# Kernel optimization log

Measured on AMD Instinct MI355X. Metric: run time of the kernel, lower is better.

Reference implementation:

```python
import jax, jax.numpy as jnp
import numpy as np
import math

BASE_RES = 16; SCALE = 1.47; N_LEVELS = 16; FDIM = 2; MAX_SPLASH = 4
LOG2 = 17; HM = 1 << LOG2; SPLITS = [0.9375, 0.875]  # sorted descending as in module


def _build_cfg():
    res = [int(BASE_RES * SCALE ** i) for i in range(N_LEVELS)]
    ns = [0] * N_LEVELS
    for i in range(N_LEVELS):
        for j, s in enumerate(SPLITS):
            if i >= N_LEVELS * s:
                ns[i] = MAX_SPLASH // (2 ** j)
                break
    nidx = [min(r ** 3, HM) for r in res]
    nfeat = [nidx[i] * max(ns[i], 1) for i in range(N_LEVELS)]
    ngau = [nidx[i] * ns[i] for i in range(N_LEVELS)]
    fb = np.concatenate([[0], np.cumsum(nfeat)]).astype(np.int64)
    gb = np.concatenate([[0], np.cumsum(ngau)]).astype(np.int64)
    return res, ns, nidx, fb, gb

RES, NS, NIDX, FB, GB = _build_cfg()
OFFS = np.array([[(k >> 2) & 1, (k >> 1) & 1, k & 1] for k in range(8)], dtype=np.int32)
PRIMES = np.array([1, 2654435761, 805459861], dtype=np.uint32)
SQRT2PI = math.sqrt(2.0 * math.pi)


def _corners_coeffs(coords, res):
    # coords: (N,3) in [0,1). Returns corners (N,8,3) int32 and trilinear coeffs (N,8).
    x = jnp.clip(res * coords, 0.0, res - 1.001)
    pos = jnp.floor(x).astype(jnp.int32)
    xf = x - pos.astype(coords.dtype)
    offs = jnp.asarray(OFFS)
    corners = pos[:, None, :] + offs[None]
    w = jnp.where(offs[None].astype(bool), xf[:, None, :], 1.0 - xf[:, None, :])
    return corners, jnp.prod(w, axis=-1)


def _hash_index(corners, res):
    # linear index if grid fits in table, else xor-prime spatial hash (mod 2^17)
    if res ** 3 <= HM:
        return corners[..., 0] + corners[..., 1] * res + corners[..., 2] * (res * res)
    c = corners.astype(jnp.uint32)
    p = jnp.asarray(PRIMES)
    h = (c[..., 0] * p[0]) ^ (c[..., 1] * p[1]) ^ (c[..., 2] * p[2])
    return (h & jnp.uint32(HM - 1)).astype(jnp.int32)


def setup_inputs() -> dict:
    key = jax.random.key(0)
    k1, k2, k3, k4 = jax.random.split(key, 4)
    N = 262144
    coords = jax.random.uniform(k1, (N, 3), dtype=jnp.float32)
    feats = 0.01 * jax.random.normal(k2, (int(FB[-1]), FDIM), dtype=jnp.float32)
    # means: uniform in a ball of radius 0.25 centered at 0.5 (init_mean)
    G = int(GB[-1])
    pts = jax.random.normal(k3, (G, 3), dtype=jnp.float32)
    r = jnp.sqrt(jax.random.uniform(jax.random.fold_in(k3, 1), (G, 1), dtype=jnp.float32))
    means = pts / jnp.linalg.norm(pts, axis=1, keepdims=True) * r * 0.25 + 0.5
    # stds: N(0.125, 0.02) as in fixed_std=False branch
    stds = 0.125 + 0.02 * jax.random.normal(k4, (G, 1), dtype=jnp.float32)
    return {"coords": coords, "feats": feats, "means": means, "stds": stds}


def reference(coords, feats, means, stds):
    out_feats = []
    out_gmm = []
    for i in range(N_LEVELS):
        res = RES[i]; ns = NS[i]
        corners, coeffs = _corners_coeffs(coords, res)  # (N,8,3), (N,8)
        idx = _hash_index(corners, res)                 # (N,8)
        f = feats[int(FB[i]):int(FB[i + 1])].reshape(-1, max(ns, 1), FDIM)[idx]  # (N,8,S,F)
        if ns:
            m = means[int(GB[i]):int(GB[i + 1])].reshape(-1, ns, 3)[idx]   # (N,8,S,3)
            s = jnp.abs(stds[int(GB[i]):int(GB[i + 1])].reshape(-1, ns, 1)[idx])  # (N,8,S,1)
            diff = coords[:, None, None, :] - m
            sq = jnp.sum(diff * diff / (2.0 * s * s + 1e-7), axis=-1, keepdims=True)
            gw = jnp.exp(-sq) / (SQRT2PI * s + 1e-7)                        # Gaussian weights
            dw = jnp.sum(jnp.abs(diff / s) ** 2, axis=-1, keepdims=True)    # normalized sq dist
            out_feats.append(jnp.einsum('nc,ncsf->nf', coeffs, gw * f))
            out_gmm.append(jnp.einsum('nc,ncs->n', coeffs, (gw * dw)[..., 0]))
        else:
            out_feats.append(jnp.einsum('nc,ncf->nf', coeffs, f[:, :, 0, :]))
    return jnp.concatenate(out_feats, axis=-1), jnp.stack(out_gmm, axis=-1)
```

## Files before the change

### kernel.cpp

```cpp
#include <hip/hip_runtime.h>
#include <math.h>


#define HMASK 131071
typedef float vf4 __attribute__((ext_vector_type(4)));
typedef float vf2 __attribute__((ext_vector_type(2)));
typedef _Float16 h8 __attribute__((ext_vector_type(8)));
typedef unsigned short u16;
typedef unsigned int u32;

#define LIN_OFF 2621440
#define L14_OFF 3670016
#define L15_OFF 7864320

__constant__ int c_fbh[10] = {180567,311639,442711,573783,704855,835927,
                              966999,1098071,1229143,1360215};
__constant__ int c_lres[4] = {16,23,34,50};
__constant__ int c_lfb[4]  = {0,4096,16263,55567};
__constant__ int c_h0res[4] = {74,109,161,237};
__constant__ int c_p1resA[3] = {348,512,753};
__constant__ int c_p1resB[3] = {1108,1629,2394};

__device__ __forceinline__ void corner_setup(int res, float cx, float cy, float cz,
                                             int& px, int& py, int& pz,
                                             float& fx, float& fy, float& fz)
{
    const float hi = (float)res - 1.001f;
    float x = fminf(fmaxf((float)res * cx, 0.0f), hi);
    float y = fminf(fmaxf((float)res * cy, 0.0f), hi);
    float z = fminf(fmaxf((float)res * cz, 0.0f), hi);
    px = (int)x; py = (int)y; pz = (int)z;
    fx = x - (float)px; fy = y - (float)py; fz = z - (float)pz;
}


__device__ __forceinline__ float2 linear_eval4(
    int res, int fbase, float cx, float cy, float cz,
    const float* __restrict__ feats)
{
    int px, py, pz; float fx, fy, fz;
    corner_setup(res, cx, cy, cz, px, py, pz, fx, fy, fz);
    int idxs[4]; float wyz[4];
#pragma unroll
    for (int j = 0; j < 4; ++j) {
        const int oy = (j >> 1) & 1, oz = j & 1;
        idxs[j] = px + (py + oy) * res + (pz + oz) * res * res;
        wyz[j] = (oy ? fy : 1.0f - fy) * (oz ? fz : 1.0f - fz);
    }
    vf4 fv[4];
#pragma unroll
    for (int j = 0; j < 4; ++j)
        fv[j] = *(const vf4*)(feats + (size_t)(fbase + idxs[j]) * 2);
    float a0 = 0.0f, a1 = 0.0f;
    const float gx = 1.0f - fx;
#pragma unroll
    for (int j = 0; j < 4; ++j) {
        a0 += wyz[j] * (gx * fv[j].x + fx * fv[j].z);
        a1 += wyz[j] * (gx * fv[j].y + fx * fv[j].w);
    }
    return make_float2(a0, a1);
}

__device__ __forceinline__ float2 plain_eval_f32h(
    int res, int fbase, float cx, float cy, float cz,
    const float* __restrict__ feats)
{
    int px, py, pz; float fx, fy, fz;
    corner_setup(res, cx, cy, cz, px, py, pz, fx, fy, fz);
    int   idxs[8];
    float ws[8];
#pragma unroll
    for (int k = 0; k < 8; ++k) {
        const int ox = (k >> 2) & 1, oy = (k >> 1) & 1, oz = k & 1;
        const int ix = px + ox, iy = py + oy, iz = pz + oz;
        ws[k] = (ox ? fx : 1.0f - fx) * (oy ? fy : 1.0f - fy) * (oz ? fz : 1.0f - fz);
        unsigned h = (unsigned)ix ^ ((unsigned)iy * 2654435761u) ^ ((unsigned)iz * 805459861u);
        idxs[k] = (int)(h & HMASK);
    }
    float2 fv[8];
#pragma unroll
    for (int k = 0; k < 8; ++k)
        fv[k] = *(const float2*)(feats + (size_t)(fbase + idxs[k]) * 2);
    float a0 = 0.0f, a1 = 0.0f;
#pragma unroll
    for (int k = 0; k < 8; ++k) { a0 += ws[k] * fv[k].x; a1 += ws[k] * fv[k].y; }
    return make_float2(a0, a1);
}


__device__ __forceinline__ float2 linear_eval4_fp8(
    int res, int ebase, float cx, float cy, float cz,
    const u32* __restrict__ ltab)
{
    int px, py, pz; float fx, fy, fz;
    corner_setup(res, cx, cy, cz, px, py, pz, fx, fy, fz);
    int idxs[4]; float wyz[4];
#pragma unroll
    for (int j = 0; j < 4; ++j) {
        const int oy = (j >> 1) & 1, oz = j & 1;
        idxs[j] = px + (py + oy) * res + (pz + oz) * res * res;
        wyz[j] = (oy ? fy : 1.0f - fy) * (oz ? fz : 1.0f - fz);
    }
    u32 u[4];
#pragma unroll
    for (int j = 0; j < 4; ++j) u[j] = ltab[ebase + idxs[j]];
    float a0 = 0.0f, a1 = 0.0f;
    const float gx = 1.0f - fx;
#pragma unroll
    for (int j = 0; j < 4; ++j) {
        vf2 lo = __builtin_amdgcn_cvt_pk_f32_fp8((int)u[j], false);
        vf2 hi = __builtin_amdgcn_cvt_pk_f32_fp8((int)u[j], true);
        a0 += wyz[j] * (gx * lo.x + fx * hi.x);
        a1 += wyz[j] * (gx * lo.y + fx * hi.y);
    }
    return make_float2(a0 * 0.0625f, a1 * 0.0625f);
}

__device__ __forceinline__ float2 plain_eval_fp8(
    int res, const u16* __restrict__ tab, float cx, float cy, float cz)
{
    int px, py, pz; float fx, fy, fz;
    corner_setup(res, cx, cy, cz, px, py, pz, fx, fy, fz);
    int   idxs[8];
    float ws[8];
#pragma unroll
    for (int k = 0; k < 8; ++k) {
        const int ox = (k >> 2) & 1, oy = (k >> 1) & 1, oz = k & 1;
        const int ix = px + ox, iy = py + oy, iz = pz + oz;
        ws[k] = (ox ? fx : 1.0f - fx) * (oy ? fy : 1.0f - fy) * (oz ? fz : 1.0f - fz);
        unsigned h = (unsigned)ix ^ ((unsigned)iy * 2654435761u) ^ ((unsigned)iz * 805459861u);
        idxs[k] = (int)(h & HMASK);
    }
    u16 v[8];
#pragma unroll
    for (int k = 0; k < 8; ++k) v[k] = tab[idxs[k]];
    float a0 = 0.0f, a1 = 0.0f;
#pragma unroll
    for (int k = 0; k < 8; ++k) {
        vf2 d = __builtin_amdgcn_cvt_pk_f32_fp8((int)v[k], false);
        a0 += ws[k] * d.x; a1 += ws[k] * d.y;
    }
    return make_float2(a0 * 0.0625f, a1 * 0.0625f);
}


__device__ __forceinline__ void gauss_pre(float w, float dx, float dy, float dz,
                                          float i2s, float inrm, float is2,
                                          float f0, float f1,
                                          float& a0, float& a1, float& ag)
{
    const float d2 = dx*dx + dy*dy + dz*dz;
    const float sq = d2 * i2s;
    const float gw = __expf(-sq) * inrm;
    const float wg = w * gw;
    a0 += wg * f0;
    a1 += wg * f1;
    ag += wg * (d2 * is2);
}

template<int NS>
__device__ __forceinline__ void splash_quarters(
    int res, const h8* __restrict__ quart, int g, int ch,
    float cx, float cy, float cz, float cox, float coy, float coz,
    float& a0, float& a1, float& ag)
{
    int px, py, pz; float fx, fy, fz;
    corner_setup(res, cx, cy, cz, px, py, pz, fx, fy, fz);
    a0 = 0.0f; a1 = 0.0f; ag = 0.0f;
#pragma unroll
    for (int j = 0; j < 4; ++j) {
        const int k = ch + 2 * j;
        const int ox = (k >> 2) & 1, oy = (k >> 1) & 1, oz = k & 1;
        const int ix = px + ox, iy = py + oy, iz = pz + oz;
        const float w = (ox ? fx : 1.0f - fx) * (oy ? fy : 1.0f - fy) * (oz ? fz : 1.0f - fz);
        unsigned h = (unsigned)ix ^ ((unsigned)iy * 2654435761u) ^ ((unsigned)iz * 805459861u);
        const int idx = (int)(h & HMASK);
        h8 Q = quart[(size_t)idx * NS + g];
        gauss_pre(w, cox - (float)Q[0], coy - (float)Q[1], coz - (float)Q[2],
                  (float)Q[3], (float)Q[4], (float)Q[5], (float)Q[6], (float)Q[7],
                  a0, a1, ag);
    }
}

template<int NS, int KN>
__device__ __forceinline__ void splash_direct_part(
    int k0, int res, int fbase, int gbase, float cx, float cy, float cz,
    const float* __restrict__ feats, const float* __restrict__ means,
    const float* __restrict__ stds, float& a0, float& a1, float& ag)
{
    int px, py, pz; float fx, fy, fz;
    corner_setup(res, cx, cy, cz, px, py, pz, fx, fy, fz);
    a0 = 0.0f; a1 = 0.0f; ag = 0.0f;
#pragma unroll
    for (int kk = 0; kk < KN; ++kk) {
        const int k = k0 + kk;
        const int ox = (k >> 2) & 1, oy = (k >> 1) & 1, oz = k & 1;
        const int ix = px + ox, iy = py + oy, iz = pz + oz;
        const float w = (ox ? fx : 1.0f - fx) * (oy ? fy : 1.0f - fy) * (oz ? fz : 1.0f - fz);
        unsigned h = (unsigned)ix ^ ((unsigned)iy * 2654435761u) ^ ((unsigned)iz * 805459861u);
        const int idx = (int)(h & HMASK);
        const int grow = gbase + idx * NS;
        const float* m = means + (size_t)grow * 3;
        const float* s = stds + grow;
        const float* f = feats + (size_t)(fbase + idx * NS) * 2;
#pragma unroll
        for (int si = 0; si < NS; ++si) {
            const float dx = cx - m[3*si], dy = cy - m[3*si+1], dz = cz - m[3*si+2];
            const float sva = fabsf(s[si]);
            const float d2 = dx*dx + dy*dy + dz*dz;
            const float s2 = sva * sva;
            const float sq = d2 / (2.0f * s2 + 1e-7f);
            const float gw = expf(-sq) / (2.5066282746310002f * sva + 1e-7f);
            const float wg = w * gw;
            a0 += wg * f[2*si];
            a1 += wg * f[2*si+1];
            ag += wg * (d2 / s2);
        }
    }
}

__global__ __launch_bounds__(256) void repack_kernel(
    const float* __restrict__ means, const float* __restrict__ stds,
    const float* __restrict__ feats, unsigned char* __restrict__ wsb)
{
    const int b = blockIdx.x;
    const int tid = threadIdx.x;
    if (b < 640) {
        const int j   = b * 256 + tid;
        const int lvl = j >> 14;
        const int e8  = (j & 16383) * 8;
        const float* src = feats + (size_t)(c_fbh[lvl] + e8) * 2;
        uint4 u;
        u32* up = (u32*)&u;
#pragma unroll
        for (int p = 0; p < 4; ++p) {
            vf4 f = *(const vf4*)(src + 4 * p);
            int w = __builtin_amdgcn_cvt_pk_fp8_f32(16.0f * f.x, 16.0f * f.y, 0, false);
            w = __builtin_amdgcn_cvt_pk_fp8_f32(16.0f * f.z, 16.0f * f.w, w, true);
            up[p] = (u32)w;
        }
        *(uint4*)(wsb + (size_t)lvl * 262144 + (size_t)e8 * 2) = u;
    } else if (b < 1346) {
        const int e = (b - 640) * 256 + tid;
        if (e < 180567) {
            const float2 fa = *(const float2*)(feats + 2 * (size_t)e);
            const float2 fb = *(const float2*)(feats + 2 * (size_t)e + 2);
            int w = __builtin_amdgcn_cvt_pk_fp8_f32(16.0f * fa.x, 16.0f * fa.y, 0, false);
            w = __builtin_amdgcn_cvt_pk_fp8_f32(16.0f * fb.x, 16.0f * fb.y, w, true);
            ((u32*)(wsb + LIN_OFF))[e] = (u32)w;
        }
    } else if (b < 1858) {
        const int e = (b - 1346) * 256 + tid;
        const float2* m2 = (const float2*)(means + (size_t)e * 6);
        const float2 ma = m2[0], mb = m2[1], mc = m2[2];
        const float2 sv = *(const float2*)(stds + 2 * e);
        const float2* f2 = (const float2*)(feats + (size_t)(1491287 + 2 * e) * 2);
        const float2 fa = f2[0], fb = f2[1];
        const float s0 = fabsf(sv.x), s1 = fabsf(sv.y);
        h8 Q0, Q1;
        Q0[0] = (_Float16)(ma.x - 0.5f); Q0[1] = (_Float16)(ma.y - 0.5f); Q0[2] = (_Float16)(mb.x - 0.5f);
        Q0[3] = (_Float16)(1.0f / (2.0f * s0 * s0 + 1e-7f));
        Q0[4] = (_Float16)(1.0f / (2.5066282746310002f * s0 + 1e-7f));
        Q0[5] = (_Float16)(1.0f / (s0 * s0));
        Q0[6] = (_Float16)fa.x; Q0[7] = (_Float16)fa.y;
        Q1[0] = (_Float16)(mb.y - 0.5f); Q1[1] = (_Float16)(mc.x - 0.5f); Q1[2] = (_Float16)(mc.y - 0.5f);
        Q1[3] = (_Float16)(1.0f / (2.0f * s1 * s1 + 1e-7f));
        Q1[4] = (_Float16)(1.0f / (2.5066282746310002f * s1 + 1e-7f));
        Q1[5] = (_Float16)(1.0f / (s1 * s1));
        Q1[6] = (_Float16)fb.x; Q1[7] = (_Float16)fb.y;
        h8* dst = (h8*)(wsb + L14_OFF) + (size_t)e * 2;
        dst[0] = Q0; dst[1] = Q1;
    } else {
        const int e = (b - 1858) * 256 + tid;
        const vf4* m4 = (const vf4*)(means + (size_t)(262144 + 4 * e) * 3);
        const vf4 u = m4[0], v = m4[1], w = m4[2];
        const vf4 s4 = *(const vf4*)(stds + 262144 + 4 * e);
        const float2* f2 = (const float2*)(feats + (size_t)(1753431 + 4 * e) * 2);
        const float2 fv[4] = {f2[0], f2[1], f2[2], f2[3]};
        const float mx[4] = {u.x, u.w, v.z, w.y};
        const float my[4] = {u.y, v.x, v.w, w.z};
        const float mz[4] = {u.z, v.y, w.x, w.w};
        const float sv[4] = {fabsf(s4.x), fabsf(s4.y), fabsf(s4.z), fabsf(s4.w)};
        h8* dst = (h8*)(wsb + L15_OFF) + (size_t)e * 4;
#pragma unroll
        for (int g = 0; g < 4; ++g) {
            h8 Q;
            Q[0] = (_Float16)(mx[g] - 0.5f);
            Q[1] = (_Float16)(my[g] - 0.5f);
            Q[2] = (_Float16)(mz[g] - 0.5f);
            Q[3] = (_Float16)(1.0f / (2.0f * sv[g] * sv[g] + 1e-7f));
            Q[4] = (_Float16)(1.0f / (2.5066282746310002f * sv[g] + 1e-7f));
            Q[5] = (_Float16)(1.0f / (sv[g] * sv[g]));
            Q[6] = (_Float16)fv[g].x; Q[7] = (_Float16)fv[g].y;
            dst[g] = Q;
        }
    }
}

template<bool PACKED>
__global__ __launch_bounds__(256) void splash_enc(
    const float* __restrict__ coords, const float* __restrict__ feats,
    const float* __restrict__ means,  const float* __restrict__ stds,
    const unsigned char* __restrict__ wsb, float* __restrict__ out, int N)
{
    const int b = blockIdx.x;
    const int tid = threadIdx.x;
    const u16* ptab = (const u16*)wsb;
    const u32* ltab = (const u32*)(wsb + LIN_OFF);
    float* gmm = out + (size_t)N * 32;

    if (b < 4096) {
        const int t = b * 256 + tid;
        const int n = t >> 2, q = t & 3;
        const float cx = coords[3*n+0], cy = coords[3*n+1], cz = coords[3*n+2];
        float2 rlin, rhsh;
        if (PACKED) {
            rlin = linear_eval4_fp8(c_lres[q], c_lfb[q], cx, cy, cz, ltab);
            rhsh = plain_eval_fp8(c_h0res[q], ptab + q * 131072, cx, cy, cz);
        } else {
            rlin = linear_eval4(c_lres[q], c_lfb[q], cx, cy, cz, feats);
            rhsh = plain_eval_f32h(c_h0res[q], c_fbh[q], cx, cy, cz, feats);
        }
        *(float2*)(out + (size_t)n * 32 + 2 * q)     = rlin;
        *(float2*)(out + (size_t)n * 32 + 8 + 2 * q) = rhsh;
    } else if (b < 7168) {
        const int t = (b - 4096) * 256 + tid;
        const int n = (int)(((unsigned long long)(unsigned)t * 0xAAAAAAABull) >> 33);
        const int q = t - 3 * n;
        const float cx = coords[3*n+0], cy = coords[3*n+1], cz = coords[3*n+2];
        float2 rA, rB;
        if (PACKED) {
            rA = plain_eval_fp8(c_p1resA[q], ptab + (4 + q) * 131072, cx, cy, cz);
            rB = plain_eval_fp8(c_p1resB[q], ptab + (7 + q) * 131072, cx, cy, cz);
        } else {
            rA = plain_eval_f32h(c_p1resA[q], c_fbh[4 + q], cx, cy, cz, feats);
            rB = plain_eval_f32h(c_p1resB[q], c_fbh[7 + q], cx, cy, cz, feats);
        }
        *(float2*)(out + (size_t)n * 32 + 16 + 2 * q) = rA;
        *(float2*)(out + (size_t)n * 32 + 22 + 2 * q) = rB;
    } else if (b < 11264) {
        const int t = (b - 7168) * 256 + tid;
        const int n = t >> 2, q = t & 3;
        const float cx = coords[3*n+0], cy = coords[3*n+1], cz = coords[3*n+2];
        float a0, a1, ag;
        if (PACKED) {
            splash_quarters<2>(3520, (const h8*)(wsb + L14_OFF), q & 1, q >> 1,
                               cx, cy, cz, cx - 0.5f, cy - 0.5f, cz - 0.5f, a0, a1, ag);
        } else {
            splash_direct_part<2,2>(q * 2, 3520, 1491287, 0, cx, cy, cz,
                                    feats, means, stds, a0, a1, ag);
        }
        a0 += __shfl_xor(a0, 1); a1 += __shfl_xor(a1, 1); ag += __shfl_xor(ag, 1);
        a0 += __shfl_xor(a0, 2); a1 += __shfl_xor(a1, 2); ag += __shfl_xor(ag, 2);
        if (q == 0) {
            *(float2*)(out + (size_t)n * 32 + 28) = make_float2(a0, a1);
            gmm[2 * n] = ag;
        }
    } else {
        const int t = (b - 11264) * 256 + tid;
        const int n = t >> 3, q = t & 7;
        const float cx = coords[3*n+0], cy = coords[3*n+1], cz = coords[3*n+2];
        float a0, a1, ag;
        if (PACKED) {
            splash_quarters<4>(5174, (const h8*)(wsb + L15_OFF), q & 3, q >> 2,
                               cx, cy, cz, cx - 0.5f, cy - 0.5f, cz - 0.5f, a0, a1, ag);
        } else {
            splash_direct_part<4,1>(q, 5174, 1753431, 262144, cx, cy, cz,
                                    feats, means, stds, a0, a1, ag);
        }
        a0 += __shfl_xor(a0, 1); a1 += __shfl_xor(a1, 1); ag += __shfl_xor(ag, 1);
        a0 += __shfl_xor(a0, 2); a1 += __shfl_xor(a1, 2); ag += __shfl_xor(ag, 2);
        a0 += __shfl_xor(a0, 4); a1 += __shfl_xor(a1, 4); ag += __shfl_xor(ag, 4);
        if (q == 0) {
            *(float2*)(out + (size_t)n * 32 + 30) = make_float2(a0, a1);
            gmm[2 * n + 1] = ag;
        }
    }
}

extern "C" void kernel_launch(void* const* d_in, const int* in_sizes, int n_in,
                              void* d_out, int out_size, void* d_ws, size_t ws_size,
                              hipStream_t stream) {
    const float* coords = (const float*)d_in[0];
    const float* feats  = (const float*)d_in[1];
    const float* means  = (const float*)d_in[2];
    const float* stds   = (const float*)d_in[3];
    float* out = (float*)d_out;
    const int N = in_sizes[0] / 3;

    const bool packed = (ws_size >= 17825792);
    if (packed) {
        repack_kernel<<<2370, 256, 0, stream>>>(means, stds, feats, (unsigned char*)d_ws);
        splash_enc<true><<<19456, 256, 0, stream>>>(coords, feats, means, stds,
                                                    (const unsigned char*)d_ws, out, N);
    } else {
        splash_enc<false><<<19456, 256, 0, stream>>>(coords, feats, means, stds,
                                                     (const unsigned char*)d_ws, out, N);
    }
}
```

Baseline: 216.8 us.

## Repack linear levels as 2x2 fp8 cells and shrink level-15 splash records

The linear-level table now stores each entry's x/y neighbours together as an 8-byte fp8 cell, so trilinear interpolation needs two loads instead of four. Level-15 Gaussian records are repacked into a 48-byte structure-of-arrays layout holding only mean, inverse-variance and features. The normalisation terms are recomputed from the inverse variance with a sqrt, and the fields are spread across lanes with shuffles, so three lanes load 16 bytes each instead of each lane loading a full 16-byte record. The goal is less gather traffic, paid for with extra shuffles, per-lane selection arithmetic, a larger workspace offset and a more expensive repack pass.

```diff
diff --git a/kernel.cpp b/kernel.cpp
--- a/kernel.cpp
+++ b/kernel.cpp
@@ -6,12 +6,13 @@
 typedef float vf4 __attribute__((ext_vector_type(4)));
 typedef float vf2 __attribute__((ext_vector_type(2)));
 typedef _Float16 h8 __attribute__((ext_vector_type(8)));
+typedef _Float16 h2 __attribute__((ext_vector_type(2)));
 typedef unsigned short u16;
 typedef unsigned int u32;
 
 #define LIN_OFF 2621440
-#define L14_OFF 3670016
-#define L15_OFF 7864320
+#define L14_OFF 4194304
+#define L15_OFF 8388608
 
 __constant__ int c_fbh[10] = {180567,311639,442711,573783,704855,835927,
                               966999,1098071,1229143,1360215};
@@ -33,6 +34,12 @@
     fx = x - (float)px; fy = y - (float)py; fz = z - (float)pz;
 }
 
+__device__ __forceinline__ float hsel_f(u32 w, int sel) {
+    h2 v;
+    __builtin_memcpy(&v, &w, 4);
+    return (float)v[sel];
+}
+
 
 __device__ __forceinline__ float2 linear_eval4(
     int res, int fbase, float cx, float cy, float cz,
@@ -88,30 +95,34 @@
 }
 
 
-__device__ __forceinline__ float2 linear_eval4_fp8(
+__device__ __forceinline__ float2 linear_eval2_fp8(
     int res, int ebase, float cx, float cy, float cz,
-    const u32* __restrict__ ltab)
+    const unsigned char* __restrict__ wsb)
 {
     int px, py, pz; float fx, fy, fz;
     corner_setup(res, cx, cy, cz, px, py, pz, fx, fy, fz);
-    int idxs[4]; float wyz[4];
-#pragma unroll
-    for (int j = 0; j < 4; ++j) {
-        const int oy = (j >> 1) & 1, oz = j & 1;
-        idxs[j] = px + (py + oy) * res + (pz + oz) * res * res;
-        wyz[j] = (oy ? fy : 1.0f - fy) * (oz ? fz : 1.0f - fz);
-    }
-    u32 u[4];
-#pragma unroll
-    for (int j = 0; j < 4; ++j) u[j] = ltab[ebase + idxs[j]];
-    float a0 = 0.0f, a1 = 0.0f;
-    const float gx = 1.0f - fx;
-#pragma unroll
-    for (int j = 0; j < 4; ++j) {
-        vf2 lo = __builtin_amdgcn_cvt_pk_f32_fp8((int)u[j], false);
-        vf2 hi = __builtin_amdgcn_cvt_pk_f32_fp8((int)u[j], true);
-        a0 += wyz[j] * (gx * lo.x + fx * hi.x);
-        a1 += wyz[j] * (gx * lo.y + fx * hi.y);
+    const int r2 = res * res;
+    const int i0 = ebase + px + py * res + pz * r2;
+    const uint2 u0 = *(const uint2*)(wsb + LIN_OFF + (size_t)i0 * 8);
+    const uint2 u1 = *(const uint2*)(wsb + LIN_OFF + (size_t)(i0 + r2) * 8);
+    const float wx0 = 1.0f - fx, wy0 = 1.0f - fy;
+    float a0, a1;
+    {
+        vf2 c00 = __builtin_amdgcn_cvt_pk_f32_fp8((int)u0.x, false);
+        vf2 c10 = __builtin_amdgcn_cvt_pk_f32_fp8((int)u0.x, true);
+        vf2 c01 = __builtin_amdgcn_cvt_pk_f32_fp8((int)u0.y, false);
+        vf2 c11 = __builtin_amdgcn_cvt_pk_f32_fp8((int)u0.y, true);
+        vf2 d00 = __builtin_amdgcn_cvt_pk_f32_fp8((int)u1.x, false);
+        vf2 d10 = __builtin_amdgcn_cvt_pk_f32_fp8((int)u1.x, true);
+        vf2 d01 = __builtin_amdgcn_cvt_pk_f32_fp8((int)u1.y, false);
+        vf2 d11 = __builtin_amdgcn_cvt_pk_f32_fp8((int)u1.y, true);
+        vf2 s0, s1;
+        s0.x = wy0 * (wx0 * c00.x + fx * c10.x) + fy * (wx0 * c01.x + fx * c11.x);
+        s0.y = wy0 * (wx0 * c00.y + fx * c10.y) + fy * (wx0 * c01.y + fx * c11.y);
+        s1.x = wy0 * (wx0 * d00.x + fx * d10.x) + fy * (wx0 * d01.x + fx * d11.x);
+        s1.y = wy0 * (wx0 * d00.y + fx * d10.y) + fy * (wx0 * d01.y + fx * d11.y);
+        a0 = (1.0f - fz) * s0.x + fz * s1.x;
+        a1 = (1.0f - fz) * s0.y + fz * s1.y;
     }
     return make_float2(a0 * 0.0625f, a1 * 0.0625f);
 }
@@ -158,14 +169,13 @@
     ag += wg * (d2 * is2);
 }
 
-template<int NS>
-__device__ __forceinline__ void splash_quarters(
-    int res, const h8* __restrict__ quart, int g, int ch,
+__device__ __forceinline__ void splash14_quarters(
+    const h8* __restrict__ quart, int g, int ch,
     float cx, float cy, float cz, float cox, float coy, float coz,
     float& a0, float& a1, float& ag)
 {
     int px, py, pz; float fx, fy, fz;
-    corner_setup(res, cx, cy, cz, px, py, pz, fx, fy, fz);
+    corner_setup(3520, cx, cy, cz, px, py, pz, fx, fy, fz);
     a0 = 0.0f; a1 = 0.0f; ag = 0.0f;
 #pragma unroll
     for (int j = 0; j < 4; ++j) {
@@ -175,10 +185,57 @@
         const float w = (ox ? fx : 1.0f - fx) * (oy ? fy : 1.0f - fy) * (oz ? fz : 1.0f - fz);
         unsigned h = (unsigned)ix ^ ((unsigned)iy * 2654435761u) ^ ((unsigned)iz * 805459861u);
         const int idx = (int)(h & HMASK);
-        h8 Q = quart[(size_t)idx * NS + g];
+        h8 Q = quart[(size_t)idx * 2 + g];
         gauss_pre(w, cox - (float)Q[0], coy - (float)Q[1], coz - (float)Q[2],
                   (float)Q[3], (float)Q[4], (float)Q[5], (float)Q[6], (float)Q[7],
                   a0, a1, ag);
+    }
+}
+
+__device__ __forceinline__ void splash15_soa(
+    int lane, float cx, float cy, float cz, float cox, float coy, float coz,
+    const unsigned char* __restrict__ wsb, float& a0, float& a1, float& ag)
+{
+    int px, py, pz; float fx, fy, fz;
+    corner_setup(5174, cx, cy, cz, px, py, pz, fx, fy, fz);
+    a0 = 0.0f; a1 = 0.0f; ag = 0.0f;
+    const int q  = lane & 7;
+    const int ch = q >> 2, g = q & 3;
+    const int B  = lane & ~3;
+    const int hdw = g >> 1;
+    const int hsel = g & 1;
+#pragma unroll
+    for (int j = 0; j < 4; ++j) {
+        const int k = ch + 2 * j;
+        const int ox = (k >> 2) & 1, oy = (k >> 1) & 1, oz = k & 1;
+        const int ix = px + ox, iy = py + oy, iz = pz + oz;
+        const float w = (ox ? fx : 1.0f - fx) * (oy ? fy : 1.0f - fy) * (oz ? fz : 1.0f - fz);
+        unsigned h = (unsigned)ix ^ ((unsigned)iy * 2654435761u) ^ ((unsigned)iz * 805459861u);
+        const int idx = (int)(h & HMASK);
+        uint4 ck = make_uint4(0u, 0u, 0u, 0u);
+        if (g < 3)
+            ck = *(const uint4*)(wsb + L15_OFF + (size_t)idx * 48 + (size_t)g * 16);
+        const u32 x01 = (u32)__shfl((int)ck.x, B,     64);
+        const u32 x23 = (u32)__shfl((int)ck.y, B,     64);
+        const u32 y01 = (u32)__shfl((int)ck.z, B,     64);
+        const u32 y23 = (u32)__shfl((int)ck.w, B,     64);
+        const u32 z01 = (u32)__shfl((int)ck.x, B + 1, 64);
+        const u32 z23 = (u32)__shfl((int)ck.y, B + 1, 64);
+        const u32 s01 = (u32)__shfl((int)ck.z, B + 1, 64);
+        const u32 s23 = (u32)__shfl((int)ck.w, B + 1, 64);
+        const u32 f001 = (u32)__shfl((int)ck.x, B + 2, 64);
+        const u32 f023 = (u32)__shfl((int)ck.y, B + 2, 64);
+        const u32 f101 = (u32)__shfl((int)ck.z, B + 2, 64);
+        const u32 f123 = (u32)__shfl((int)ck.w, B + 2, 64);
+        const float mx  = hsel_f(hdw ? x23 : x01, hsel);
+        const float my  = hsel_f(hdw ? y23 : y01, hsel);
+        const float mz  = hsel_f(hdw ? z23 : z01, hsel);
+        const float i2s = hsel_f(hdw ? s23 : s01, hsel);
+        const float f0  = hsel_f(hdw ? f023 : f001, hsel);
+        const float f1  = hsel_f(hdw ? f123 : f101, hsel);
+        const float inrm = __fsqrt_rn(i2s * 0.31830988618f);
+        const float is2  = 2.0f * i2s;
+        gauss_pre(w, cox - mx, coy - my, coz - mz, i2s, inrm, is2, f0, f1, a0, a1, ag);
     }
 }
 
@@ -219,6 +276,28 @@
     }
 }
 
+
+template<int RES>
+__device__ __forceinline__ void pack_lin_xy(
+    int e, int lfb, const float* __restrict__ feats, unsigned char* __restrict__ wsb)
+{
+    const int local = e - lfb;
+    const int px = local % RES;
+    const int t  = local / RES;
+    const int py = t % RES;
+    const int dx = (px + 1 < RES) ? 1 : 0;
+    const int dy = (py + 1 < RES) ? RES : 0;
+    const float2 f00 = *(const float2*)(feats + 2 * (size_t)e);
+    const float2 f10 = *(const float2*)(feats + 2 * (size_t)(e + dx));
+    const float2 f01 = *(const float2*)(feats + 2 * (size_t)(e + dy));
+    const float2 f11 = *(const float2*)(feats + 2 * (size_t)(e + dx + dy));
+    int w0 = __builtin_amdgcn_cvt_pk_fp8_f32(16.0f * f00.x, 16.0f * f00.y, 0, false);
+    w0 = __builtin_amdgcn_cvt_pk_fp8_f32(16.0f * f10.x, 16.0f * f10.y, w0, true);
+    int w1 = __builtin_amdgcn_cvt_pk_fp8_f32(16.0f * f01.x, 16.0f * f01.y, 0, false);
+    w1 = __builtin_amdgcn_cvt_pk_fp8_f32(16.0f * f11.x, 16.0f * f11.y, w1, true);
+    *(uint2*)(wsb + LIN_OFF + (size_t)e * 8) = make_uint2((u32)w0, (u32)w1);
+}
+
 __global__ __launch_bounds__(256) void repack_kernel(
     const float* __restrict__ means, const float* __restrict__ stds,
     const float* __restrict__ feats, unsigned char* __restrict__ wsb)
@@ -243,11 +322,10 @@
     } else if (b < 1346) {
         const int e = (b - 640) * 256 + tid;
         if (e < 180567) {
-            const float2 fa = *(const float2*)(feats + 2 * (size_t)e);
-            const float2 fb = *(const float2*)(feats + 2 * (size_t)e + 2);
-            int w = __builtin_amdgcn_cvt_pk_fp8_f32(16.0f * fa.x, 16.0f * fa.y, 0, false);
-            w = __builtin_amdgcn_cvt_pk_fp8_f32(16.0f * fb.x, 16.0f * fb.y, w, true);
-            ((u32*)(wsb + LIN_OFF))[e] = (u32)w;
+            if (e < 4096)       pack_lin_xy<16>(e, 0,     feats, wsb);
+            else if (e < 16263) pack_lin_xy<23>(e, 4096,  feats, wsb);
+            else if (e < 55567) pack_lin_xy<34>(e, 16263, feats, wsb);
+            else                pack_lin_xy<50>(e, 55567, feats, wsb);
         }
     } else if (b < 1858) {
         const int e = (b - 1346) * 256 + tid;
@@ -281,19 +359,20 @@
         const float my[4] = {u.y, v.x, v.w, w.z};
         const float mz[4] = {u.z, v.y, w.x, w.w};
         const float sv[4] = {fabsf(s4.x), fabsf(s4.y), fabsf(s4.z), fabsf(s4.w)};
-        h8* dst = (h8*)(wsb + L15_OFF) + (size_t)e * 4;
+        h8 C0, C1, C2;
 #pragma unroll
         for (int g = 0; g < 4; ++g) {
-            h8 Q;
-            Q[0] = (_Float16)(mx[g] - 0.5f);
-            Q[1] = (_Float16)(my[g] - 0.5f);
-            Q[2] = (_Float16)(mz[g] - 0.5f);
-            Q[3] = (_Float16)(1.0f / (2.0f * sv[g] * sv[g] + 1e-7f));
-            Q[4] = (_Float16)(1.0f / (2.5066282746310002f * sv[g] + 1e-7f));
-            Q[5] = (_Float16)(1.0f / (sv[g] * sv[g]));
-            Q[6] = (_Float16)fv[g].x; Q[7] = (_Float16)fv[g].y;
-            dst[g] = Q;
-        }
+            C0[g]     = (_Float16)(mx[g] - 0.5f);
+            C0[4 + g] = (_Float16)(my[g] - 0.5f);
+            C1[g]     = (_Float16)(mz[g] - 0.5f);
+            C1[4 + g] = (_Float16)(1.0f / (2.0f * sv[g] * sv[g] + 1e-7f));
+            C2[g]     = (_Float16)fv[g].x;
+            C2[4 + g] = (_Float16)fv[g].y;
+        }
+        unsigned char* dst = wsb + L15_OFF + (size_t)e * 48;
+        *(h8*)(dst)      = C0;
+        *(h8*)(dst + 16) = C1;
+        *(h8*)(dst + 32) = C2;
     }
 }
 
@@ -306,7 +385,6 @@
     const int b = blockIdx.x;
     const int tid = threadIdx.x;
     const u16* ptab = (const u16*)wsb;
-    const u32* ltab = (const u32*)(wsb + LIN_OFF);
     float* gmm = out + (size_t)N * 32;
 
     if (b < 4096) {
@@ -315,7 +393,7 @@
         const float cx = coords[3*n+0], cy = coords[3*n+1], cz = coords[3*n+2];
         float2 rlin, rhsh;
         if (PACKED) {
-            rlin = linear_eval4_fp8(c_lres[q], c_lfb[q], cx, cy, cz, ltab);
+            rlin = linear_eval2_fp8(c_lres[q], c_lfb[q], cx, cy, cz, wsb);
             rhsh = plain_eval_fp8(c_h0res[q], ptab + q * 131072, cx, cy, cz);
         } else {
             rlin = linear_eval4(c_lres[q], c_lfb[q], cx, cy, cz, feats);
@@ -344,8 +422,8 @@
         const float cx = coords[3*n+0], cy = coords[3*n+1], cz = coords[3*n+2];
         float a0, a1, ag;
         if (PACKED) {
-            splash_quarters<2>(3520, (const h8*)(wsb + L14_OFF), q & 1, q >> 1,
-                               cx, cy, cz, cx - 0.5f, cy - 0.5f, cz - 0.5f, a0, a1, ag);
+            splash14_quarters((const h8*)(wsb + L14_OFF), q & 1, q >> 1,
+                              cx, cy, cz, cx - 0.5f, cy - 0.5f, cz - 0.5f, a0, a1, ag);
         } else {
             splash_direct_part<2,2>(q * 2, 3520, 1491287, 0, cx, cy, cz,
                                     feats, means, stds, a0, a1, ag);
@@ -362,8 +440,8 @@
         const float cx = coords[3*n+0], cy = coords[3*n+1], cz = coords[3*n+2];
         float a0, a1, ag;
         if (PACKED) {
-            splash_quarters<4>(5174, (const h8*)(wsb + L15_OFF), q & 3, q >> 2,
-                               cx, cy, cz, cx - 0.5f, cy - 0.5f, cz - 0.5f, a0, a1, ag);
+            splash15_soa(tid & 63, cx, cy, cz, cx - 0.5f, cy - 0.5f, cz - 0.5f,
+                         wsb, a0, a1, ag);
         } else {
             splash_direct_part<4,1>(q, 5174, 1753431, 262144, cx, cy, cz,
                                     feats, means, stds, a0, a1, ag);
```

After: 208.4 us. 1.04x faster.
